# Kernel optimization log

Measured on AMD Instinct MI355X. Metric: run time of the kernel, lower is better.

Reference implementation:

```python
import jax, jax.numpy as jnp
import numpy as np
from jax import lax

NUM_CLASSES = 10
NUM_ITERS = 3


def conv2d(x, w, b, stride):
    # x: [B,C,H,W], w: [O,I,kh,kw]
    y = lax.conv_general_dilated(x, w, (stride, stride), 'VALID',
                                 dimension_numbers=('NCHW', 'OIHW', 'NCHW'))
    return y + b[None, :, None, None]


def squash(t, axis=-1):
    sn = jnp.sum(t * t, axis=axis, keepdims=True)
    return (sn / (1.0 + sn)) * t / jnp.sqrt(sn)


def routing(x, W, num_iters=NUM_ITERS):
    # x: [B,R,Ci], W: [C,R,Ci,Co] -> outputs [B,C,Co]
    # priors[c,b,r,o] = sum_i x[b,r,i] * W[c,r,i,o]
    priors = jnp.einsum('bri,crio->cbro', x, W)  # [C,B,R,Co]
    C, B, R, Co = priors.shape
    # torch logits are [C,B,R,1,Co] but identical along Co (zeros init,
    # delta broadcast), so a [C,B,R,1] logit is mathematically identical.
    logits = jnp.zeros((C, B, R, 1), priors.dtype)
    outputs = None
    for i in range(num_iters):
        probs = jax.nn.softmax(logits, axis=2)            # over route nodes
        s = jnp.sum(probs * priors, axis=2, keepdims=True)  # [C,B,1,Co]
        outputs = squash(s, axis=-1)
        if i != num_iters - 1:
            logits = logits + jnp.sum(priors * outputs, axis=-1, keepdims=True)
    return jnp.transpose(outputs[:, :, 0, :], (1, 0, 2))  # [B,C,Co]


def setup_inputs() -> dict:
    key = jax.random.key(0)
    ks = jax.random.split(key, 16)
    B = 32
    s = 0.05
    inp = {
        'x': jax.random.normal(ks[0], (B, 1, 61, 61), jnp.float32),
        'conv0_w': jax.random.normal(ks[1], (256, 1, 9, 9), jnp.float32) * s,
        'conv0_b': jnp.zeros((256,), jnp.float32),
        'conv1_w': jax.random.normal(ks[2], (256, 256, 9, 9), jnp.float32) * s,
        'conv1_b': jnp.zeros((256,), jnp.float32),
        # 8 primary-capsule convs stacked: [8*32, 256, 9, 9]
        'prim_w': jax.random.normal(ks[3], (8 * 32, 256, 9, 9), jnp.float32) * s,
        'prim_b': jnp.zeros((8 * 32,), jnp.float32),
        'W1': jax.random.normal(ks[4], (64, 32 * 6 * 6, 8, 16), jnp.float32) * s,
        'W2': jax.random.normal(ks[5], (NUM_CLASSES, 64, 16, 16), jnp.float32) * s,
        'dec_w1': jax.random.normal(ks[6], (16 * NUM_CLASSES, 1024), jnp.float32) * s,
        'dec_b1': jnp.zeros((1024,), jnp.float32),
        'dec_w2': jax.random.normal(ks[7], (1024, 2048), jnp.float32) * s,
        'dec_b2': jnp.zeros((2048,), jnp.float32),
        'dec_w3': jax.random.normal(ks[8], (2048, 4096), jnp.float32) * s,
        'dec_b3': jnp.zeros((4096,), jnp.float32),
    }
    return inp


def reference(x, conv0_w, conv0_b, conv1_w, conv1_b, prim_w, prim_b,
              W1, W2, dec_w1, dec_b1, dec_w2, dec_b2, dec_w3, dec_b3):
    B = x.shape[0]
    h = jax.nn.relu(conv2d(x, conv0_w, conv0_b, 2))       # [B,256,27,27]
    h = jax.nn.relu(conv2d(h, conv1_w, conv1_b, 1))       # [B,256,19,19]
    # primary capsules: 8 convs of 32 channels each, k9 s2 -> [B,256,6,6]
    p = conv2d(h, prim_w, prim_b, 2)
    # torch: each capsule conv -> view(B, 32*6*6, 1), cat on last -> [B,1152,8]
    p = p.reshape(B, 8, 32 * 6 * 6)                        # [B,8,1152]
    p = jnp.transpose(p, (0, 2, 1))                        # [B,1152,8]
    p = squash(p, axis=-1)
    u = routing(p, W1)                                     # [B,64,16]
    v = routing(u, W2)                                     # [B,10,16]
    classes = jnp.sqrt(jnp.sum(v * v, axis=-1))            # [B,10]
    classes = jax.nn.softmax(classes, axis=-1)
    y = jax.nn.one_hot(jnp.argmax(classes, axis=1), NUM_CLASSES,
                       dtype=v.dtype)                       # [B,10]
    y = lax.stop_gradient(y)
    z = (v * y[:, :, None]).reshape(B, -1)                 # [B,160]
    d = jax.nn.relu(z @ dec_w1 + dec_b1)
    d = jax.nn.relu(d @ dec_w2 + dec_b2)
    reconstructions = jax.nn.sigmoid(d @ dec_w3 + dec_b3)  # [B,4096]
    return classes, reconstructions
```

## Files before the change

kernel.cpp:

```cpp
#include <hip/hip_runtime.h>
#include <hip/hip_bf16.h>
#include <math.h>


#define NB 32

typedef _Float16 f16;
typedef f16 f16x2 __attribute__((ext_vector_type(2)));
typedef f16 f16x4 __attribute__((ext_vector_type(4)));
typedef f16 f16x8 __attribute__((ext_vector_type(8)));
typedef float f32x4 __attribute__((ext_vector_type(4)));

__device__ __forceinline__ int swz(int row, int q) {
  return row * 64 + ((q * 16) ^ (((row >> 1) & 3) << 4));
}

__global__ __launch_bounds__(256) void wprep_kernel(
    const float* __restrict__ w1, const float* __restrict__ w2,
    f16* __restrict__ wo1, f16* __restrict__ wo2) {
  __shared__ f16 tile[256][82];
  int bi = blockIdx.x;
  const float* src;
  f16* dst;
  if (bi < 256) {
    src = w1 + (size_t)bi * 20736;
    dst = wo1 + bi * 256;
  } else {
    src = w2 + (size_t)(bi - 256) * 20736;
    dst = wo2 + (bi - 256) * 256;
  }
  int t = threadIdx.x;
  for (int j = t; j < 20736; j += 256) {
    int r = j / 81, c = j - r * 81;
    tile[r][c] = (f16)src[j];
  }
  __syncthreads();
  f16* d = dst + t;
  for (int tap = 0; tap < 81; ++tap)
    d[(size_t)tap * 65536] = tile[t][tap];
}

__global__ __launch_bounds__(256) void conv0_kernel(
    const float* __restrict__ x, const float* __restrict__ w,
    const float* __restrict__ bias, f16* __restrict__ outf) {
  int b = blockIdx.x, ocg = blockIdx.y, z = blockIdx.z;
  __shared__ float img[61 * 61];
  __shared__ __align__(16) float wl[81][32];
  int t = threadIdx.x;
  for (int i = t; i < 61 * 61; i += 256) img[i] = x[b * 3721 + i];
  for (int i = t; i < 81 * 32; i += 256) {
    int k = i >> 5, oc = i & 31;
    wl[k][oc] = w[(ocg * 32 + oc) * 81 + k];
  }
  __syncthreads();
  int ocs = (t & 7) * 4;
  int pg  = t >> 3;
  int oc0 = ocg * 32 + ocs;
  float b0 = bias[oc0 + 0], b1 = bias[oc0 + 1], b2 = bias[oc0 + 2],
        b3 = bias[oc0 + 3];
  for (int p = pg + z * 32; p < 729; p += 64) {
    int oh = p / 27, ow = p - oh * 27;
    float a0 = 0.f, a1 = 0.f, a2 = 0.f, a3 = 0.f;
    const float* ib = &img[oh * 2 * 61 + ow * 2];
#pragma unroll
    for (int kh = 0; kh < 9; ++kh) {
#pragma unroll
      for (int kw = 0; kw < 9; ++kw) {
        float v = ib[kh * 61 + kw];
        const float4 wv =
            *reinterpret_cast<const float4*>(&wl[kh * 9 + kw][ocs]);
        a0 += v * wv.x; a1 += v * wv.y; a2 += v * wv.z; a3 += v * wv.w;
      }
    }
    int po = oh * 28 + ow;
    f16x4 hv;
    hv[0] = (f16)fmaxf(a0 + b0, 0.f);
    hv[1] = (f16)fmaxf(a1 + b1, 0.f);
    hv[2] = (f16)fmaxf(a2 + b2, 0.f);
    hv[3] = (f16)fmaxf(a3 + b3, 0.f);
    *(f16x4*)&outf[((size_t)b * 756 + po) * 256 + oc0] = hv;
  }
}

__global__ __launch_bounds__(256, 3) void conv1_mfma(
    const f16* __restrict__ xin,
    const f16* __restrict__ wA,
    f16* __restrict__ part) {
  int f = blockIdx.x;
  int v = f & 7, j = f >> 3;
  int slice = v * 2 + (j >> 6);
  int within = j & 63;
  int ph = within >> 5, b = within & 31;
  int ocg = slice & 3, ksp = slice >> 2;
  __shared__ __align__(16) f16 blds[504 * 32];
  __shared__ __align__(16) f16 alds[2][64 * 32];
  int t = threadIdx.x;
  int w = t >> 6, lane = t & 63, kg = lane >> 4, ln = lane & 15;
  int aoc = t >> 2, aq = t & 3;
  int row0 = ph * 252;
  int prow[3];
#pragma unroll
  for (int nf = 0; nf < 3; ++nf) {
    int n = ph * 192 + w * 48 + nf * 16 + ln;
    int oh = n / 20, ow = n - oh * 20;
    if (oh > 18) oh = 18;
    if (ow > 18) ow = 18;
    prow[nf] = oh * 28 + ow - row0;
  }
  f32x4 acc[4][3];
#pragma unroll
  for (int m = 0; m < 4; ++m)
#pragma unroll
    for (int nf = 0; nf < 3; ++nf) acc[m][nf] = (f32x4){0.f, 0.f, 0.f, 0.f};

  const f16* xb = xin + (size_t)b * 756 * 256 + ksp * 64;
  const f16* ab = wA + (size_t)(ocg * 64 + aoc) * 256 + ksp * 64 + aq * 8;
  for (int icc = 0; icc < 2; ++icc) {
    __syncthreads();
    for (int i = t; i < 2016; i += 256) {
      int p = i >> 2, q = i & 3;
      f16x8 val =
          *(const f16x8*)(xb + (size_t)(row0 + p) * 256 + icc * 32 + q * 8);
      *(f16x8*)((char*)blds + swz(p, q)) = val;
    }
    {
      f16x8 val = *(const f16x8*)(ab + icc * 32);
      *(f16x8*)((char*)alds[0] + swz(aoc, aq)) = val;
    }
    __syncthreads();
    for (int tap = 0; tap < 81; ++tap) {
      int cur = tap & 1;
      if (tap < 80) {
        f16x8 val = *(const f16x8*)(ab + (size_t)(tap + 1) * 65536 + icc * 32);
        *(f16x8*)((char*)alds[cur ^ 1] + swz(aoc, aq)) = val;
      }
      int kh = tap / 9, kw = tap - kh * 9;
      int shift = kh * 28 + kw;
      f16x8 af[4];
#pragma unroll
      for (int m = 0; m < 4; ++m)
        af[m] = *(const f16x8*)((const char*)alds[cur] + swz(m * 16 + ln, kg));
      f16x8 bf[3];
#pragma unroll
      for (int nf = 0; nf < 3; ++nf)
        bf[nf] =
            *(const f16x8*)((const char*)blds + swz(prow[nf] + shift, kg));
#pragma unroll
      for (int m = 0; m < 4; ++m)
#pragma unroll
        for (int nf = 0; nf < 3; ++nf)
          acc[m][nf] = __builtin_amdgcn_mfma_f32_16x16x32_f16(
              af[m], bf[nf], acc[m][nf], 0, 0, 0);
      __syncthreads();
    }
  }
  f16* pout = part + ((size_t)ksp * 32 + b) * 384 * 256 + ocg * 64;
#pragma unroll
  for (int m = 0; m < 4; ++m)
#pragma unroll
    for (int nf = 0; nf < 3; ++nf) {
      int n = ph * 192 + w * 48 + nf * 16 + ln;
      int oc = m * 16 + kg * 4;
      f16x4 val;
#pragma unroll
      for (int jj = 0; jj < 4; ++jj) val[jj] = (f16)acc[m][nf][jj];
      *(f16x4*)(pout + (size_t)n * 256 + oc) = val;
    }
}

__global__ void comb1_kernel(const f16* __restrict__ part,
                             const float* __restrict__ bias,
                             f16* __restrict__ h1f) {
  int idx = blockIdx.x * 256 + threadIdx.x;
  if (idx >= 32 * 380 * 32) return;
  int ocq = idx & 31, rem = idx >> 5;
  int p = rem % 380, b = rem / 380;
  float a[8];
#pragma unroll
  for (int j = 0; j < 8; ++j) a[j] = bias[ocq * 8 + j];
#pragma unroll
  for (int k = 0; k < 4; ++k) {
    f16x8 v = *(const f16x8*)&part[(((size_t)k * 32 + b) * 384 + p) * 256 +
                                   ocq * 8];
#pragma unroll
    for (int j = 0; j < 8; ++j) a[j] += (float)v[j];
  }
  f16x8 o;
#pragma unroll
  for (int j = 0; j < 8; ++j) o[j] = (f16)fmaxf(a[j], 0.f);
  *(f16x8*)&h1f[((size_t)b * 380 + p) * 256 + ocq * 8] = o;
}

__global__ __launch_bounds__(256, 3) void prim_mfma(
    const f16* __restrict__ xin,
    const f16* __restrict__ wB,
    float* __restrict__ part2) {
  int f = blockIdx.x;
  int v = f & 7, j = f >> 3;
  int slice = v * 2 + (j >> 5);
  int b = j & 31;
  int ocg = slice & 1, ksp = slice >> 1;
  __shared__ __align__(16) f16 blds[384 * 32];
  __shared__ __align__(16) f16 alds[2][128 * 32];
  int t = threadIdx.x;
  int w = t >> 6, lane = t & 63, kg = lane >> 4, ln = lane & 15;
  int rbase[3];
#pragma unroll
  for (int nf = 0; nf < 3; ++nf) {
    int rem = nf * 16 + ln;
    int oh6 = rem >> 3, ow6 = rem & 7;
    rbase[nf] = oh6 * 40 + ow6 * 2;
  }
  f32x4 acc[2][3];
#pragma unroll
  for (int m = 0; m < 2; ++m)
#pragma unroll
    for (int nf = 0; nf < 3; ++nf) acc[m][nf] = (f32x4){0.f, 0.f, 0.f, 0.f};

  for (int i = t; i < 1536; i += 256) {
    int pos = i >> 2, q = i & 3;
    int p = pos < 380 ? pos : pos - 20;
    f16x8 val = *(const f16x8*)(xin + ((size_t)b * 380 + p) * 256 + ksp * 32 +
                                q * 8);
    *(f16x8*)((char*)blds + swz(pos, q)) = val;
  }
  const f16* ab = wB + (size_t)(ocg * 128) * 256 + ksp * 32;
  for (int i = t; i < 512; i += 256) {
    int oc = i >> 2, q = i & 3;
    f16x8 val = *(const f16x8*)(ab + (size_t)oc * 256 + q * 8);
    *(f16x8*)((char*)alds[0] + swz(oc, q)) = val;
  }
  __syncthreads();
  for (int tap = 0; tap < 81; ++tap) {
    int cur = tap & 1;
    if (tap < 80) {
      for (int i = t; i < 512; i += 256) {
        int oc = i >> 2, q = i & 3;
        f16x8 val = *(const f16x8*)(ab + (size_t)(tap + 1) * 65536 +
                                    (size_t)oc * 256 + q * 8);
        *(f16x8*)((char*)alds[cur ^ 1] + swz(oc, q)) = val;
      }
    }
    int kh = tap / 9, kw = tap - kh * 9;
    int shift = kh * 20 + kw;
    f16x8 af[2];
#pragma unroll
    for (int m = 0; m < 2; ++m)
      af[m] = *(const f16x8*)((const char*)alds[cur] +
                              swz((w * 2 + m) * 16 + ln, kg));
    f16x8 bf[3];
#pragma unroll
    for (int nf = 0; nf < 3; ++nf)
      bf[nf] = *(const f16x8*)((const char*)blds + swz(rbase[nf] + shift, kg));
#pragma unroll
    for (int m = 0; m < 2; ++m)
#pragma unroll
      for (int nf = 0; nf < 3; ++nf)
        acc[m][nf] = __builtin_amdgcn_mfma_f32_16x16x32_f16(
            af[m], bf[nf], acc[m][nf], 0, 0, 0);
    __syncthreads();
  }
  float* pout = part2 + ((size_t)ksp * 32 + b) * 48 * 256 + ocg * 128;
#pragma unroll
  for (int m = 0; m < 2; ++m)
#pragma unroll
    for (int nf = 0; nf < 3; ++nf) {
      int n = nf * 16 + ln;
      int oc = (w * 2 + m) * 16 + kg * 4;
      *(f32x4*)(pout + (size_t)n * 256 + oc) = acc[m][nf];
    }
}

__global__ __launch_bounds__(256) void combsq_kernel(
    const float* __restrict__ part2,
    const float* __restrict__ bias, float* __restrict__ caps) {
  int bn = blockIdx.x;
  int b = bn / 48, n = bn - b * 48;
  int ow6 = n & 7;
  if (ow6 >= 6) return;
  int oh6 = n >> 3, s = oh6 * 6 + ow6;
  __shared__ float al[256];
  int oc = threadIdx.x;
  float a = 0.f;
#pragma unroll
  for (int k = 0; k < 8; ++k)
    a += part2[(((size_t)k * 32 + b) * 48 + n) * 256 + oc];
  al[oc] = a;
  __syncthreads();
  if (oc < 32) {
    int m = oc;
    float tv[8];
    float sn = 0.f;
#pragma unroll
    for (int g = 0; g < 8; ++g) {
      float v = al[g * 32 + m] + bias[g * 32 + m];
      tv[g] = v;
      sn += v * v;
    }
    float sc = sqrtf(sn) / (1.f + sn);
#pragma unroll
    for (int g = 0; g < 8; ++g)
      caps[((size_t)b * 1152 + m * 36 + s) * 8 + g] = tv[g] * sc;
  }
}

__global__ __launch_bounds__(256) void priors1_kernel(
    const float* __restrict__ x,
    const float* __restrict__ W,
    f16* __restrict__ pri) {
  int c = blockIdx.x, rt = blockIdx.y;
  int r0 = rt * 32;
  __shared__ __align__(16) float xl[32 * 32 * 8];
  int t = threadIdx.x;
  for (int q = t; q < 2048; q += 256) {
    int b = q >> 6, j = q & 63;
    *(float4*)&xl[b * 256 + j * 4] =
        *(const float4*)&x[(size_t)b * 9216 + r0 * 8 + j * 4];
  }
  int rl = t >> 3, oq = t & 7;
  float w0[8], w1[8];
#pragma unroll
  for (int i = 0; i < 8; ++i) {
    const float2 wv = *(const float2*)&W[
        (((size_t)c * 1152 + r0 + rl) * 8 + i) * 16 + 2 * oq];
    w0[i] = wv.x; w1[i] = wv.y;
  }
  __syncthreads();
  f16* pout = pri + (size_t)c * 32 * 18432 + (r0 + rl) * 16 + 2 * oq;
#pragma unroll 4
  for (int b = 0; b < 32; ++b) {
    const float4 x0 = *(const float4*)&xl[b * 256 + rl * 8];
    const float4 x1 = *(const float4*)&xl[b * 256 + rl * 8 + 4];
    float s0 = x0.x * w0[0] + x0.y * w0[1] + x0.z * w0[2] + x0.w * w0[3] +
               x1.x * w0[4] + x1.y * w0[5] + x1.z * w0[6] + x1.w * w0[7];
    float s1 = x0.x * w1[0] + x0.y * w1[1] + x0.z * w1[2] + x0.w * w1[3] +
               x1.x * w1[4] + x1.y * w1[5] + x1.z * w1[6] + x1.w * w1[7];
    f16x2 hv; hv[0] = (f16)s0; hv[1] = (f16)s1;
    *(f16x2*)(pout + (size_t)b * 18432) = hv;
  }
}

__global__ __launch_bounds__(512) void route1_kernel(
    const f16* __restrict__ pri,
    float* __restrict__ out) {
  constexpr int R = 1152;
  constexpr int NREG = 36;
  int c = blockIdx.x, b = blockIdx.y;
  __shared__ float lg[R], pr[R];
  __shared__ float redA[8], redB[8];
  __shared__ float sred[8][16];
  __shared__ float vsh[17];
  int t    = threadIdx.x;
  int o    = t & 15;
  int rhi  = t >> 4;
  int wid  = t >> 6;
  int lane = t & 63;
  const f16* pb = pri + ((size_t)c * 32 + b) * (R * 16);

  float prireg[NREG];
#pragma unroll
  for (int k = 0; k < NREG; ++k)
    prireg[k] = (float)pb[(k * 32 + rhi) * 16 + o];
  for (int r = t; r < R; r += 512) lg[r] = 0.f;
  __syncthreads();

  for (int it = 0; it < 3; ++it) {
    float lm = -1e30f;
    for (int r = t; r < R; r += 512) lm = fmaxf(lm, lg[r]);
#pragma unroll
    for (int s2 = 1; s2 <= 32; s2 <<= 1) lm = fmaxf(lm, __shfl_xor(lm, s2));
    if (lane == 0) redA[wid] = lm;
    __syncthreads();
    if (t == 0) {
      float m8 = redA[0];
#pragma unroll
      for (int w = 1; w < 8; ++w) m8 = fmaxf(m8, redA[w]);
      redA[0] = m8;
    }
    __syncthreads();
    float m = redA[0];
    float ls = 0.f;
    for (int r = t; r < R; r += 512) {
      float e = __expf(lg[r] - m);
      pr[r] = e;
      ls += e;
    }
#pragma unroll
    for (int s2 = 1; s2 <= 32; s2 <<= 1) ls += __shfl_xor(ls, s2);
    if (lane == 0) redB[wid] = ls;
    __syncthreads();
    if (t == 0) {
      float s8 = 0.f;
#pragma unroll
      for (int w = 0; w < 8; ++w) s8 += redB[w];
      redB[0] = s8;
    }
    __syncthreads();
    float denom = redB[0];
    float part = 0.f;
#pragma unroll
    for (int k = 0; k < NREG; ++k) part += pr[k * 32 + rhi] * prireg[k];
    part += __shfl_xor(part, 16);
    part += __shfl_xor(part, 32);
    if (lane < 16) sred[wid][lane] = part;
    __syncthreads();
    if (t < 16) {
      float sv = 0.f;
#pragma unroll
      for (int w = 0; w < 8; ++w) sv += sred[w][t];
      vsh[t] = sv / denom;
    }
    __syncthreads();
    if (t == 0) {
      float sn = 0.f;
#pragma unroll
      for (int oo = 0; oo < 16; ++oo) sn += vsh[oo] * vsh[oo];
      vsh[16] = sqrtf(sn) / (1.f + sn);
    }
    __syncthreads();
    if (it < 2) {
      float vo = vsh[o] * vsh[16];
#pragma unroll
      for (int k = 0; k < NREG; ++k) {
        float val = prireg[k] * vo;
        val += __shfl_xor(val, 1);
        val += __shfl_xor(val, 2);
        val += __shfl_xor(val, 4);
        val += __shfl_xor(val, 8);
        if (o == 0) lg[k * 32 + rhi] += val;
      }
      __syncthreads();
    }
  }
  if (t < 16) out[((size_t)b * 64 + c) * 16 + t] = vsh[t] * vsh[16];
}

template <int R, int CI>
__global__ __launch_bounds__(512) void routing_kernel(
    const float* __restrict__ x,
    const float* __restrict__ W,
    float* __restrict__ out) {
  constexpr int NREG = R * 16 / 512;
  int c = blockIdx.x, b = blockIdx.y;
  int C = gridDim.x;
  __shared__ float xls[R * CI];
  extern __shared__ float rdyn[];
  float* lg = rdyn;
  float* pr = rdyn + R;
  __shared__ float redA[8], redB[8];
  __shared__ float sred[8][16];
  __shared__ float vsh[17];
  int t    = threadIdx.x;
  int o    = t & 15;
  int rhi  = t >> 4;
  int wid  = t >> 6;
  int lane = t & 63;
  const float* xb = x + (size_t)b * R * CI;
  const float* Wc = W + (size_t)c * R * CI * 16;

  for (int i = t; i < R * CI; i += 512) xls[i] = xb[i];
  for (int r = t; r < R; r += 512) lg[r] = 0.f;
  __syncthreads();

  float pri[NREG];
#pragma unroll
  for (int k = 0; k < NREG; ++k) {
    int r = k * 32 + rhi;
    float s = 0.f;
#pragma unroll
    for (int i = 0; i < CI; ++i)
      s += xls[r * CI + i] * Wc[((size_t)r * CI + i) * 16 + o];
    pri[k] = s;
  }

  for (int it = 0; it < 3; ++it) {
    float lm = -1e30f;
    for (int r = t; r < R; r += 512) lm = fmaxf(lm, lg[r]);
#pragma unroll
    for (int s2 = 1; s2 <= 32; s2 <<= 1) lm = fmaxf(lm, __shfl_xor(lm, s2));
    if (lane == 0) redA[wid] = lm;
    __syncthreads();
    if (t == 0) {
      float m8 = redA[0];
#pragma unroll
      for (int w = 1; w < 8; ++w) m8 = fmaxf(m8, redA[w]);
      redA[0] = m8;
    }
    __syncthreads();
    float m = redA[0];
    float ls = 0.f;
    for (int r = t; r < R; r += 512) {
      float e = __expf(lg[r] - m);
      pr[r] = e;
      ls += e;
    }
#pragma unroll
    for (int s2 = 1; s2 <= 32; s2 <<= 1) ls += __shfl_xor(ls, s2);
    if (lane == 0) redB[wid] = ls;
    __syncthreads();
    if (t == 0) {
      float s8 = 0.f;
#pragma unroll
      for (int w = 0; w < 8; ++w) s8 += redB[w];
      redB[0] = s8;
    }
    __syncthreads();
    float denom = redB[0];
    float part = 0.f;
#pragma unroll
    for (int k = 0; k < NREG; ++k) part += pr[k * 32 + rhi] * pri[k];
    part += __shfl_xor(part, 16);
    part += __shfl_xor(part, 32);
    if (lane < 16) sred[wid][lane] = part;
    __syncthreads();
    if (t < 16) {
      float sv = 0.f;
#pragma unroll
      for (int w = 0; w < 8; ++w) sv += sred[w][t];
      vsh[t] = sv / denom;
    }
    __syncthreads();
    if (t == 0) {
      float sn = 0.f;
#pragma unroll
      for (int oo = 0; oo < 16; ++oo) sn += vsh[oo] * vsh[oo];
      vsh[16] = sqrtf(sn) / (1.f + sn);
    }
    __syncthreads();
    if (it < 2) {
      float vo = vsh[o] * vsh[16];
#pragma unroll
      for (int k = 0; k < NREG; ++k) {
        float val = pri[k] * vo;
        val += __shfl_xor(val, 1);
        val += __shfl_xor(val, 2);
        val += __shfl_xor(val, 4);
        val += __shfl_xor(val, 8);
        if (o == 0) lg[k * 32 + rhi] += val;
      }
      __syncthreads();
    }
  }
  if (t < 16) out[((size_t)b * C + c) * 16 + t] = vsh[t] * vsh[16];
}

__global__ void classes_kernel(const float* __restrict__ v,
                               float* __restrict__ outc,
                               int* __restrict__ amaxb) {
  int b = blockIdx.x;
  int t = threadIdx.x;
  __shared__ float nrm[10];
  if (t < 10) {
    float sn = 0.f;
#pragma unroll
    for (int o = 0; o < 16; ++o) {
      float xv = v[(b * 10 + t) * 16 + o];
      sn += xv * xv;
    }
    nrm[t] = sqrtf(sn);
  }
  __syncthreads();
  if (t == 0) {
    float m = nrm[0];
    int am = 0;
    for (int c = 1; c < 10; ++c)
      if (nrm[c] > m) { m = nrm[c]; am = c; }
    float s = 0.f;
    float e[10];
    for (int c = 0; c < 10; ++c) { e[c] = __expf(nrm[c] - m); s += e[c]; }
    for (int c = 0; c < 10; ++c) outc[b * 10 + c] = e[c] / s;
    amaxb[b] = am;
  }
}

__global__ __launch_bounds__(256) void fc1s_kernel(
    const float* __restrict__ v, const int* __restrict__ amaxb,
    const float* __restrict__ w, const float* __restrict__ bias,
    float* __restrict__ out) {
  int n  = blockIdx.x * 256 + threadIdx.x;
  int b0 = blockIdx.y * 8;
  __shared__ float vls[8][16];
  __shared__ int ams[8];
  int t = threadIdx.x;
  if (t < 8) ams[t] = amaxb[b0 + t];
  __syncthreads();
  if (t < 128) {
    int bb = t >> 4, oo = t & 15;
    vls[bb][oo] = v[((b0 + bb) * 10 + ams[bb]) * 16 + oo];
  }
  __syncthreads();
  float bv = bias[n];
#pragma unroll
  for (int bb = 0; bb < 8; ++bb) {
    int row0 = ams[bb] * 16;
    float acc = bv;
#pragma unroll
    for (int oo = 0; oo < 16; ++oo)
      acc += vls[bb][oo] * w[(size_t)(row0 + oo) * 1024 + n];
    out[(size_t)(b0 + bb) * 1024 + n] = fmaxf(acc, 0.f);
  }
}

template <int K, int KCH>
__global__ __launch_bounds__(256) void fcsplit_kernel(
    const float* __restrict__ in, const float* __restrict__ w,
    float* __restrict__ pbuf, int N) {
  int n  = blockIdx.x * 256 + threadIdx.x;
  int b0 = blockIdx.y * 8;
  int k0 = blockIdx.z * KCH;
  __shared__ __align__(16) float inl[KCH * 8];
  for (int idx = threadIdx.x; idx < 8 * KCH; idx += 256) {
    int bb = idx / KCH, k = idx - bb * KCH;
    inl[k * 8 + bb] = in[(size_t)(b0 + bb) * K + k0 + k];
  }
  __syncthreads();
  float acc[8];
#pragma unroll
  for (int bb = 0; bb < 8; ++bb) acc[bb] = 0.f;
  for (int k = 0; k < KCH; ++k) {
    float wv = w[(size_t)(k0 + k) * N + n];
    const float4 i0 = *reinterpret_cast<const float4*>(&inl[k * 8]);
    const float4 i1 = *reinterpret_cast<const float4*>(&inl[k * 8 + 4]);
    acc[0] += i0.x * wv; acc[1] += i0.y * wv;
    acc[2] += i0.z * wv; acc[3] += i0.w * wv;
    acc[4] += i1.x * wv; acc[5] += i1.y * wv;
    acc[6] += i1.z * wv; acc[7] += i1.w * wv;
  }
#pragma unroll
  for (int bb = 0; bb < 8; ++bb)
    pbuf[((size_t)blockIdx.z * 32 + b0 + bb) * N + n] = acc[bb];
}

template <int KS, bool RELU, bool SIG>
__global__ void fccomb_kernel(const float* __restrict__ pbuf,
                              const float* __restrict__ bias,
                              float* __restrict__ out, int N) {
  int idx = blockIdx.x * 256 + threadIdx.x;
  if (idx >= 32 * N) return;
  int b = idx / N, n = idx - b * N;
  float a = bias[n];
#pragma unroll
  for (int kz = 0; kz < KS; ++kz) a += pbuf[((size_t)kz * 32 + b) * N + n];
  if (RELU) a = fmaxf(a, 0.f);
  if (SIG)  a = 1.f / (1.f + __expf(-a));
  out[idx] = a;
}

extern "C" void kernel_launch(void* const* d_in, const int* in_sizes, int n_in,
                              void* d_out, int out_size, void* d_ws,
                              size_t ws_size, hipStream_t stream) {
  const float* x       = (const float*)d_in[0];
  const float* conv0_w = (const float*)d_in[1];
  const float* conv0_b = (const float*)d_in[2];
  const float* conv1_w = (const float*)d_in[3];
  const float* conv1_b = (const float*)d_in[4];
  const float* prim_w  = (const float*)d_in[5];
  const float* prim_b  = (const float*)d_in[6];
  const float* W1      = (const float*)d_in[7];
  const float* W2      = (const float*)d_in[8];
  const float* dec_w1  = (const float*)d_in[9];
  const float* dec_b1  = (const float*)d_in[10];
  const float* dec_w2  = (const float*)d_in[11];
  const float* dec_b2  = (const float*)d_in[12];
  const float* dec_w3  = (const float*)d_in[13];
  const float* dec_b3  = (const float*)d_in[14];
  float* out = (float*)d_out;

  float* ws    = (float*)d_ws;
  float* caps  = ws;
  float* u     = caps + 294912;
  float* vc    = u + 32768;
  int*   amaxb = (int*)(vc + 5120);
  float* trans = vc + 5120 + 32;

  f16* wA    = (f16*)trans;
  f16* wB    = wA + 5308416;
  f16* h0f   = wB + 5308416;
  f16* h1f   = h0f + 6193152;
  f16* part1 = h1f + 3112960;
  float* part2 = (float*)part1;
  f16* pri1  = (f16*)trans;
  float* d1  = trans;
  float* d2  = d1 + 32768;
  float* pb2 = d2 + 65536;
  float* pb3 = pb2 + 262144;

  wprep_kernel<<<512, 256, 0, stream>>>(conv1_w, prim_w, wA, wB);

  conv0_kernel<<<dim3(NB, 8, 2), 256, 0, stream>>>(x, conv0_w, conv0_b, h0f);

  conv1_mfma<<<1024, 256, 0, stream>>>(h0f, wA, part1);
  comb1_kernel<<<1520, 256, 0, stream>>>(part1, conv1_b, h1f);

  prim_mfma<<<512, 256, 0, stream>>>(h1f, wB, part2);
  combsq_kernel<<<NB * 48, 256, 0, stream>>>(part2, prim_b, caps);

  priors1_kernel<<<dim3(64, 36), 256, 0, stream>>>(caps, W1, pri1);
  route1_kernel<<<dim3(64, NB), 512, 0, stream>>>(pri1, u);

  routing_kernel<64, 16>
      <<<dim3(10, NB), 512, 2 * 64 * sizeof(float), stream>>>(u, W2, vc);

  classes_kernel<<<NB, 64, 0, stream>>>(vc, out, amaxb);

  fc1s_kernel<<<dim3(4, 4), 256, 0, stream>>>(vc, amaxb, dec_w1, dec_b1, d1);

  fcsplit_kernel<1024, 256>
      <<<dim3(8, 4, 4), 256, 0, stream>>>(d1, dec_w2, pb2, 2048);
  fccomb_kernel<4, true, false>
      <<<256, 256, 0, stream>>>(pb2, dec_b2, d2, 2048);

  fcsplit_kernel<2048, 256>
      <<<dim3(16, 4, 8), 256, 0, stream>>>(d2, dec_w3, pb3, 4096);
  fccomb_kernel<8, false, true>
      <<<512, 256, 0, stream>>>(pb3, dec_b3, out + 320, 4096);
}
```

Measured before the change: 441.3 us.

## Widen conv1 MFMA per-wave tile, specialize first routing iteration, fuse classes into fc1

The conv1 MFMA kernel now runs 128 threads per block, and each wave computes 6 N-fragments instead of 3. Each A fragment is reused across more MFMAs and the per-block LDS fill is shared by fewer waves, at the cost of more accumulator registers and lower occupancy. Both routing kernels skip the softmax in the first iteration, since uniform logits make the probabilities exactly 1/R, so a plain mean is used instead. The classes kernel is folded into the first decoder FC kernel, which removes one launch and the argmax buffer but repeats the norm computation in every block.

```diff
diff --git a/kernel.cpp b/kernel.cpp
--- a/kernel.cpp
+++ b/kernel.cpp
@@ -82,7 +82,7 @@
   }
 }
 
-__global__ __launch_bounds__(256, 3) void conv1_mfma(
+__global__ __launch_bounds__(128, 2) void conv1_mfma(
     const f16* __restrict__ xin,
     const f16* __restrict__ wA,
     f16* __restrict__ part) {
@@ -96,43 +96,50 @@
   __shared__ __align__(16) f16 alds[2][64 * 32];
   int t = threadIdx.x;
   int w = t >> 6, lane = t & 63, kg = lane >> 4, ln = lane & 15;
-  int aoc = t >> 2, aq = t & 3;
   int row0 = ph * 252;
-  int prow[3];
-#pragma unroll
-  for (int nf = 0; nf < 3; ++nf) {
-    int n = ph * 192 + w * 48 + nf * 16 + ln;
+  int prow[6];
+#pragma unroll
+  for (int nf = 0; nf < 6; ++nf) {
+    int n = ph * 192 + w * 96 + nf * 16 + ln;
     int oh = n / 20, ow = n - oh * 20;
     if (oh > 18) oh = 18;
     if (ow > 18) ow = 18;
     prow[nf] = oh * 28 + ow - row0;
   }
-  f32x4 acc[4][3];
+  f32x4 acc[4][6];
 #pragma unroll
   for (int m = 0; m < 4; ++m)
 #pragma unroll
-    for (int nf = 0; nf < 3; ++nf) acc[m][nf] = (f32x4){0.f, 0.f, 0.f, 0.f};
+    for (int nf = 0; nf < 6; ++nf) acc[m][nf] = (f32x4){0.f, 0.f, 0.f, 0.f};
 
   const f16* xb = xin + (size_t)b * 756 * 256 + ksp * 64;
-  const f16* ab = wA + (size_t)(ocg * 64 + aoc) * 256 + ksp * 64 + aq * 8;
+  const f16* ab = wA + (size_t)(ocg * 64) * 256 + ksp * 64;
   for (int icc = 0; icc < 2; ++icc) {
     __syncthreads();
-    for (int i = t; i < 2016; i += 256) {
+    for (int i = t; i < 2016; i += 128) {
       int p = i >> 2, q = i & 3;
       f16x8 val =
           *(const f16x8*)(xb + (size_t)(row0 + p) * 256 + icc * 32 + q * 8);
       *(f16x8*)((char*)blds + swz(p, q)) = val;
     }
-    {
-      f16x8 val = *(const f16x8*)(ab + icc * 32);
+#pragma unroll
+    for (int i = t; i < 256; i += 128) {
+      int aoc = i >> 2, aq = i & 3;
+      f16x8 val =
+          *(const f16x8*)(ab + (size_t)aoc * 256 + icc * 32 + aq * 8);
       *(f16x8*)((char*)alds[0] + swz(aoc, aq)) = val;
     }
     __syncthreads();
     for (int tap = 0; tap < 81; ++tap) {
       int cur = tap & 1;
       if (tap < 80) {
-        f16x8 val = *(const f16x8*)(ab + (size_t)(tap + 1) * 65536 + icc * 32);
-        *(f16x8*)((char*)alds[cur ^ 1] + swz(aoc, aq)) = val;
+#pragma unroll
+        for (int i = t; i < 256; i += 128) {
+          int aoc = i >> 2, aq = i & 3;
+          f16x8 val = *(const f16x8*)(ab + (size_t)(tap + 1) * 65536 +
+                                      (size_t)aoc * 256 + icc * 32 + aq * 8);
+          *(f16x8*)((char*)alds[cur ^ 1] + swz(aoc, aq)) = val;
+        }
       }
       int kh = tap / 9, kw = tap - kh * 9;
       int shift = kh * 28 + kw;
@@ -140,15 +147,15 @@
 #pragma unroll
       for (int m = 0; m < 4; ++m)
         af[m] = *(const f16x8*)((const char*)alds[cur] + swz(m * 16 + ln, kg));
-      f16x8 bf[3];
-#pragma unroll
-      for (int nf = 0; nf < 3; ++nf)
+      f16x8 bf[6];
+#pragma unroll
+      for (int nf = 0; nf < 6; ++nf)
         bf[nf] =
             *(const f16x8*)((const char*)blds + swz(prow[nf] + shift, kg));
 #pragma unroll
       for (int m = 0; m < 4; ++m)
 #pragma unroll
-        for (int nf = 0; nf < 3; ++nf)
+        for (int nf = 0; nf < 6; ++nf)
           acc[m][nf] = __builtin_amdgcn_mfma_f32_16x16x32_f16(
               af[m], bf[nf], acc[m][nf], 0, 0, 0);
       __syncthreads();
@@ -158,8 +165,8 @@
 #pragma unroll
   for (int m = 0; m < 4; ++m)
 #pragma unroll
-    for (int nf = 0; nf < 3; ++nf) {
-      int n = ph * 192 + w * 48 + nf * 16 + ln;
+    for (int nf = 0; nf < 6; ++nf) {
+      int n = ph * 192 + w * 96 + nf * 16 + ln;
       int oc = m * 16 + kg * 4;
       f16x4 val;
 #pragma unroll
@@ -361,10 +368,42 @@
 #pragma unroll
   for (int k = 0; k < NREG; ++k)
     prireg[k] = (float)pb[(k * 32 + rhi) * 16 + o];
-  for (int r = t; r < R; r += 512) lg[r] = 0.f;
-  __syncthreads();
-
-  for (int it = 0; it < 3; ++it) {
+
+  {
+    float part = 0.f;
+#pragma unroll
+    for (int k = 0; k < NREG; ++k) part += prireg[k];
+    part += __shfl_xor(part, 16);
+    part += __shfl_xor(part, 32);
+    if (lane < 16) sred[wid][lane] = part;
+    __syncthreads();
+    if (t < 16) {
+      float sv = 0.f;
+#pragma unroll
+      for (int w = 0; w < 8; ++w) sv += sred[w][t];
+      vsh[t] = sv / (float)R;
+    }
+    __syncthreads();
+    if (t == 0) {
+      float sn = 0.f;
+#pragma unroll
+      for (int oo = 0; oo < 16; ++oo) sn += vsh[oo] * vsh[oo];
+      vsh[16] = sqrtf(sn) / (1.f + sn);
+    }
+    __syncthreads();
+    float vo = vsh[o] * vsh[16];
+#pragma unroll
+    for (int k = 0; k < NREG; ++k) {
+      float val = prireg[k] * vo;
+      val += __shfl_xor(val, 1);
+      val += __shfl_xor(val, 2);
+      val += __shfl_xor(val, 4);
+      val += __shfl_xor(val, 8);
+      if (o == 0) lg[k * 32 + rhi] = val;
+    }
+    __syncthreads();
+  }
+  for (int it = 1; it < 3; ++it) {
     float lm = -1e30f;
     for (int r = t; r < R; r += 512) lm = fmaxf(lm, lg[r]);
 #pragma unroll
@@ -459,7 +498,6 @@
   const float* Wc = W + (size_t)c * R * CI * 16;
 
   for (int i = t; i < R * CI; i += 512) xls[i] = xb[i];
-  for (int r = t; r < R; r += 512) lg[r] = 0.f;
   __syncthreads();
 
   float pri[NREG];
@@ -473,7 +511,41 @@
     pri[k] = s;
   }
 
-  for (int it = 0; it < 3; ++it) {
+  {
+    float part = 0.f;
+#pragma unroll
+    for (int k = 0; k < NREG; ++k) part += pri[k];
+    part += __shfl_xor(part, 16);
+    part += __shfl_xor(part, 32);
+    if (lane < 16) sred[wid][lane] = part;
+    __syncthreads();
+    if (t < 16) {
+      float sv = 0.f;
+#pragma unroll
+      for (int w = 0; w < 8; ++w) sv += sred[w][t];
+      vsh[t] = sv / (float)R;
+    }
+    __syncthreads();
+    if (t == 0) {
+      float sn = 0.f;
+#pragma unroll
+      for (int oo = 0; oo < 16; ++oo) sn += vsh[oo] * vsh[oo];
+      vsh[16] = sqrtf(sn) / (1.f + sn);
+    }
+    __syncthreads();
+    float vo = vsh[o] * vsh[16];
+#pragma unroll
+    for (int k = 0; k < NREG; ++k) {
+      float val = pri[k] * vo;
+      val += __shfl_xor(val, 1);
+      val += __shfl_xor(val, 2);
+      val += __shfl_xor(val, 4);
+      val += __shfl_xor(val, 8);
+      if (o == 0) lg[k * 32 + rhi] = val;
+    }
+    __syncthreads();
+  }
+  for (int it = 1; it < 3; ++it) {
     float lm = -1e30f;
     for (int r = t; r < R; r += 512) lm = fmaxf(lm, lg[r]);
 #pragma unroll
@@ -544,49 +616,44 @@
   if (t < 16) out[((size_t)b * C + c) * 16 + t] = vsh[t] * vsh[16];
 }
 
-__global__ void classes_kernel(const float* __restrict__ v,
-                               float* __restrict__ outc,
-                               int* __restrict__ amaxb) {
-  int b = blockIdx.x;
-  int t = threadIdx.x;
-  __shared__ float nrm[10];
-  if (t < 10) {
-    float sn = 0.f;
-#pragma unroll
-    for (int o = 0; o < 16; ++o) {
-      float xv = v[(b * 10 + t) * 16 + o];
-      sn += xv * xv;
-    }
-    nrm[t] = sqrtf(sn);
-  }
-  __syncthreads();
-  if (t == 0) {
-    float m = nrm[0];
-    int am = 0;
-    for (int c = 1; c < 10; ++c)
-      if (nrm[c] > m) { m = nrm[c]; am = c; }
-    float s = 0.f;
-    float e[10];
-    for (int c = 0; c < 10; ++c) { e[c] = __expf(nrm[c] - m); s += e[c]; }
-    for (int c = 0; c < 10; ++c) outc[b * 10 + c] = e[c] / s;
-    amaxb[b] = am;
-  }
-}
-
-__global__ __launch_bounds__(256) void fc1s_kernel(
-    const float* __restrict__ v, const int* __restrict__ amaxb,
-    const float* __restrict__ w, const float* __restrict__ bias,
+__global__ __launch_bounds__(256) void fc1cls_kernel(
+    const float* __restrict__ v, const float* __restrict__ w,
+    const float* __restrict__ bias, float* __restrict__ outc,
     float* __restrict__ out) {
   int n  = blockIdx.x * 256 + threadIdx.x;
   int b0 = blockIdx.y * 8;
-  __shared__ float vls[8][16];
+  int t = threadIdx.x;
+  __shared__ float vall[8][160];
+  __shared__ float nrm[8][10];
   __shared__ int ams[8];
-  int t = threadIdx.x;
-  if (t < 8) ams[t] = amaxb[b0 + t];
-  __syncthreads();
-  if (t < 128) {
-    int bb = t >> 4, oo = t & 15;
-    vls[bb][oo] = v[((b0 + bb) * 10 + ams[bb]) * 16 + oo];
+  for (int idx = t; idx < 1280; idx += 256) {
+    int bb = idx / 160, j = idx - bb * 160;
+    vall[bb][j] = v[(size_t)(b0 + bb) * 160 + j];
+  }
+  __syncthreads();
+  if (t < 80) {
+    int bb = t / 10, c = t - bb * 10;
+    float sn = 0.f;
+#pragma unroll
+    for (int o = 0; o < 16; ++o) {
+      float xv = vall[bb][c * 16 + o];
+      sn += xv * xv;
+    }
+    nrm[bb][c] = sqrtf(sn);
+  }
+  __syncthreads();
+  if (t < 8) {
+    float m = nrm[t][0];
+    int am = 0;
+    for (int c = 1; c < 10; ++c)
+      if (nrm[t][c] > m) { m = nrm[t][c]; am = c; }
+    ams[t] = am;
+    if (blockIdx.x == 0) {
+      float s = 0.f;
+      float e[10];
+      for (int c = 0; c < 10; ++c) { e[c] = __expf(nrm[t][c] - m); s += e[c]; }
+      for (int c = 0; c < 10; ++c) outc[(b0 + t) * 10 + c] = e[c] / s;
+    }
   }
   __syncthreads();
   float bv = bias[n];
@@ -596,7 +663,7 @@
     float acc = bv;
 #pragma unroll
     for (int oo = 0; oo < 16; ++oo)
-      acc += vls[bb][oo] * w[(size_t)(row0 + oo) * 1024 + n];
+      acc += vall[bb][row0 + oo] * w[(size_t)(row0 + oo) * 1024 + n];
     out[(size_t)(b0 + bb) * 1024 + n] = fmaxf(acc, 0.f);
   }
 }
@@ -670,7 +737,6 @@
   float* caps  = ws;
   float* u     = caps + 294912;
   float* vc    = u + 32768;
-  int*   amaxb = (int*)(vc + 5120);
   float* trans = vc + 5120 + 32;
 
   f16* wA    = (f16*)trans;
@@ -689,7 +755,7 @@
 
   conv0_kernel<<<dim3(NB, 8, 2), 256, 0, stream>>>(x, conv0_w, conv0_b, h0f);
 
-  conv1_mfma<<<1024, 256, 0, stream>>>(h0f, wA, part1);
+  conv1_mfma<<<1024, 128, 0, stream>>>(h0f, wA, part1);
   comb1_kernel<<<1520, 256, 0, stream>>>(part1, conv1_b, h1f);
 
   prim_mfma<<<512, 256, 0, stream>>>(h1f, wB, part2);
@@ -701,9 +767,7 @@
   routing_kernel<64, 16>
       <<<dim3(10, NB), 512, 2 * 64 * sizeof(float), stream>>>(u, W2, vc);
 
-  classes_kernel<<<NB, 64, 0, stream>>>(vc, out, amaxb);
-
-  fc1s_kernel<<<dim3(4, 4), 256, 0, stream>>>(vc, amaxb, dec_w1, dec_b1, d1);
+  fc1cls_kernel<<<dim3(4, 4), 256, 0, stream>>>(vc, dec_w1, dec_b1, out, d1);
 
   fcsplit_kernel<1024, 256>
       <<<dim3(8, 4, 4), 256, 0, stream>>>(d1, dec_w2, pb2, 2048);
```

New measurement: 485.3 us. 1.1x slower.
